# Kernel tuning notes

Hardware: AMD Instinct MI355X
Metric: run time of the kernel (lower is better)

## Reference

```python
import jax, jax.numpy as jnp
import numpy as np

M_FEATS = 1536      # number of proposals (docstring: [M, K])
K_DIM = 128         # feature dim per docstring example
NUM_CLASSES = 16    # label vocabulary; torch.unique loop becomes a fixed class sweep


def setup_inputs() -> dict:
    key = jax.random.key(0)
    k1, k2 = jax.random.split(key)
    features = jax.random.normal(k1, (M_FEATS, K_DIM), dtype=jnp.float32)
    labels = jax.random.randint(k2, (M_FEATS,), 0, NUM_CLASSES, dtype=jnp.int32)
    # ious all ones -> keep = (ious >= 0.5) is all-True, so the boolean filter is identity
    ious = jnp.ones((M_FEATS,), dtype=jnp.float32)
    return {"features": features, "labels": labels, "ious": ious}


def reference(features, labels, ious):
    # reweight_func='none' -> coef = ones_like(ious); keep mask is all-True by construction
    coef = jnp.ones_like(ious)
    # similarity [M, M]; coef broadcasts over columns, matching `similarity * coef` in torch
    sim = jnp.matmul(features, features.T) * coef[None, :]
    m = sim.shape[0]
    eye = jnp.eye(m, dtype=sim.dtype)
    # ground set term: logdet(similarity + 0.5 I)  (mask_ground is all ones)
    ground = jnp.linalg.slogdet(sim + 0.5 * eye)[1]

    # Per-label logdet of the submatrix S_c + 0.5 I_{n_c}. Instead of extracting a
    # variable-size submatrix (not jit-able), embed it in a full [M, M] matrix that is
    # block-diagonal: class block = S_c + 0.5 I, off-class diagonal = 1. Its logdet
    # equals logdet(S_c + 0.5 I). Absent classes give identity -> logdet 0, matching
    # torch.unique skipping them.
    onehot = (labels[:, None] == jnp.arange(NUM_CLASSES, dtype=labels.dtype)[None, :])
    onehot = onehot.astype(sim.dtype)  # [M, C]

    def class_logdet(mask):  # mask: [M] 0/1 indicator for one class
        A = sim * (mask[:, None] * mask[None, :]) + jnp.diag(0.5 * mask + (1.0 - mask))
        return jnp.linalg.slogdet(A)[1]

    per_class = jax.vmap(class_logdet)(onehot.T)  # [C]
    loss = jnp.sum(per_class) - ground
    return loss  # scalar; .mean() of a scalar is itself
```

## Files before the change

kernel.cpp:

```cpp
#include <hip/hip_runtime.h>
#include <math.h>


#define M_FEATS 1536
#define K_DIM 128
#define NUM_CLASSES 16
#define GRAM_ELEMS (K_DIM * K_DIM)
#define SENT 0x13579BDF
#define MP 104
#define ALD 132
#define WS 24

typedef short bf16x8 __attribute__((ext_vector_type(8)));
typedef float f32x4 __attribute__((ext_vector_type(4)));

__device__ __forceinline__ short f2bf(float x) {
    unsigned u = __float_as_uint(x);
    u += 0x7FFFu + ((u >> 16) & 1u);
    return (short)(u >> 16);
}

__device__ __forceinline__ float chol128_mfma(
    const int t, const float* __restrict__ Agram, float* __restrict__ strip,
    short* __restrict__ Whl, float* __restrict__ logp)
{
    const int wave = t >> 6, lane = t & 63, ln = lane & 15, quad = lane >> 4;

    f32x4 acc[2][8];
#pragma unroll
    for (int x = 0; x < 2; ++x)
#pragma unroll
        for (int tc = 0; tc < 8; ++tc)
            acc[x][tc] = (f32x4){0.f, 0.f, 0.f, 0.f};

#pragma unroll 1
    for (int s = 0; s < 16; ++s) {
        const int k = 8 * s;

        const int sb = s >> 1, sw = sb >> 1, sx = sb & 1, sq = (s & 1) * 2;
        if (wave == sw && (quad == sq || quad == sq + 1)) {
            const int qrel = quad - sq;
            const int rbase = (sw * 2 + sx) * 16 + quad * 4;
            if (sx == 0) {
#pragma unroll
                for (int tc = 0; tc < 8; ++tc)
#pragma unroll
                    for (int rr = 0; rr < 4; ++rr)
                        strip[(qrel * 4 + rr) * 128 + tc * 16 + ln] =
                            Agram[(rbase + rr) * ALD + tc * 16 + ln] - acc[0][tc][rr];
            } else {
#pragma unroll
                for (int tc = 0; tc < 8; ++tc)
#pragma unroll
                    for (int rr = 0; rr < 4; ++rr)
                        strip[(qrel * 4 + rr) * 128 + tc * 16 + ln] =
                            Agram[(rbase + rr) * ALD + tc * 16 + ln] - acc[1][tc][rr];
            }
        }
        __syncthreads();

        if (t < K_DIM) {
            float D[8][8];
#pragma unroll
            for (int r = 0; r < 8; ++r) {
                float4 d0 = *(const float4*)(strip + r * 128 + k);
                float4 d1 = *(const float4*)(strip + r * 128 + k + 4);
                D[r][0] = d0.x; D[r][1] = d0.y; D[r][2] = d0.z; D[r][3] = d0.w;
                D[r][4] = d1.x; D[r][5] = d1.y; D[r][6] = d1.z; D[r][7] = d1.w;
            }
            float a[8];
#pragma unroll
            for (int c = 0; c < 8; ++c) a[c] = strip[c * 128 + t];

            float L[8][8], ic[8];
            float prod = 1.0f;
#pragma unroll
            for (int c = 0; c < 8; ++c) {
                float v = D[c][c];
#pragma unroll
                for (int m = 0; m < c; ++m) v = fmaf(-L[c][m], L[c][m], v);
                prod *= v;
                ic[c] = rsqrtf(v);
#pragma unroll
                for (int r = c + 1; r < 8; ++r) {
                    float x = D[r][c];
#pragma unroll
                    for (int m = 0; m < c; ++m) x = fmaf(-L[r][m], L[c][m], x);
                    L[r][c] = x * ic[c];
                }
            }
            if (t == 0) logp[s] = prod;

            float w[8];
#pragma unroll
            for (int c = 0; c < 8; ++c) {
                float x = a[c];
#pragma unroll
                for (int m = 0; m < c; ++m) x = fmaf(-L[c][m], w[m], x);
                w[c] = x * ic[c];
            }
            if (t < k) {
#pragma unroll
                for (int c = 0; c < 8; ++c) w[c] = 0.f;
            }

            unsigned uh[4], ul[4];
#pragma unroll
            for (int j = 0; j < 4; ++j) {
                const float w0 = w[2 * j], w1 = w[2 * j + 1];
                const unsigned h0 = (unsigned short)f2bf(w0);
                const unsigned h1 = (unsigned short)f2bf(w1);
                const float f0 = __uint_as_float(h0 << 16);
                const float f1 = __uint_as_float(h1 << 16);
                const unsigned l0 = (unsigned short)f2bf(w0 - f0);
                const unsigned l1 = (unsigned short)f2bf(w1 - f1);
                uh[j] = (h1 << 16) | h0;
                ul[j] = (l1 << 16) | l0;
            }
            *(int4*)(Whl + t * WS) =
                make_int4((int)uh[0], (int)uh[1], (int)uh[2], (int)uh[3]);
            *(int4*)(Whl + t * WS + 8) =
                make_int4((int)ul[0], (int)ul[1], (int)ul[2], (int)ul[3]);
        }
        __syncthreads();

        const int live = 8 * (s + 1);
        const bool live0 = ((wave * 2 + 0) * 16 + 16) > live;
        const bool live1 = ((wave * 2 + 1) * 16 + 16) > live;
        if (live0 | live1) {
            const bf16x8 z = {};
            const short* a0p = Whl + (((wave * 2 + 0) * 16 + ln) * WS) + (quad & 1) * 8;
            const short* a1p = Whl + (((wave * 2 + 1) * 16 + ln) * WS) + (quad & 1) * 8;
            bf16x8 a0 = *(const bf16x8*)a0p;
            bf16x8 a1 = *(const bf16x8*)a1p;
            a0 = (quad < 2) ? a0 : z;
            a1 = (quad < 2) ? a1 : z;
#pragma unroll
            for (int tc = 0; tc < 8; ++tc) {
                if ((tc * 16 + 16) <= live) continue;
                const short* bp = Whl + (tc * 16 + ln) * WS;
                bf16x8 bh = *(const bf16x8*)(bp);
                bf16x8 bl = *(const bf16x8*)(bp + 8);
                bh = (quad < 2) ? bh : z;
                bl = (quad < 2) ? bl : z;
                if (live0) {
                    acc[0][tc] = __builtin_amdgcn_mfma_f32_16x16x32_bf16(
                        a0, bh, acc[0][tc], 0, 0, 0);
                    acc[0][tc] = __builtin_amdgcn_mfma_f32_16x16x32_bf16(
                        a0, bl, acc[0][tc], 0, 0, 0);
                }
                if (live1) {
                    acc[1][tc] = __builtin_amdgcn_mfma_f32_16x16x32_bf16(
                        a1, bh, acc[1][tc], 0, 0, 0);
                    acc[1][tc] = __builtin_amdgcn_mfma_f32_16x16x32_bf16(
                        a1, bl, acc[1][tc], 0, 0, 0);
                }
            }
        }
    }

    float ls = 0.0f;
    if (t == 0) {
#pragma unroll
        for (int ss = 0; ss < 16; ++ss) ls += logf(logp[ss]);
    }
    return ls;
}

__global__ __launch_bounds__(256, 1) void fused_kernel(
    const float* __restrict__ f, const int* __restrict__ labels,
    float* __restrict__ groundG, float* __restrict__ ldet,
    int* __restrict__ flagG, int* __restrict__ flag3,
    float* __restrict__ out)
{
    __shared__ int cnt;
    __shared__ int list[M_FEATS];
    __shared__ __align__(16) short FT[K_DIM * MP];
    __shared__ __align__(16) float Agram[K_DIM * ALD];
    __shared__ __align__(16) float strip[8 * 128];
    __shared__ __align__(16) short Whl[K_DIM * WS];
    __shared__ float logp[16];

    const int b = blockIdx.x;
    const int t = threadIdx.x;

    if (b < NUM_CLASSES) {
        const int cls = b;
        if (t == 0) cnt = 0;
        __syncthreads();
        {
            const int lane = t & 63;
            const unsigned long long ltmask = (lane == 63)
                ? 0x7FFFFFFFFFFFFFFFull : ((1ull << lane) - 1ull);
#pragma unroll
            for (int it = 0; it < M_FEATS / 256; ++it) {
                const int i = it * 256 + t;
                const bool pred = (labels[i] == cls);
                const unsigned long long mask = __ballot(pred);
                int base = 0;
                if (lane == 0 && mask)
                    base = atomicAdd(&cnt, __popcll(mask));
                base = __shfl(base, 0);
                if (pred)
                    list[base + __popcll(mask & ltmask)] = i;
            }
        }
        __syncthreads();
        const int n = cnt;

        const int wave = t >> 6, lane = t & 63, ln = lane & 15, quad = lane >> 4;
        const int mlane = t & 31, cgrp = t >> 5;

        f32x4 acc[2][8];
#pragma unroll
        for (int x = 0; x < 2; ++x)
#pragma unroll
            for (int tc = 0; tc < 8; ++tc)
                acc[x][tc] = (f32x4){0.f, 0.f, 0.f, 0.f};

        const int nchunks = (n + 95) / 96;
        for (int ch = 0; ch < nchunks; ++ch) {
            const int cb = ch * 96;
#pragma unroll
            for (int it = 0; it < 12; ++it) {
                const int m = (it % 3) * 32 + mlane;
                const int cgp = (it / 3) * 8 + cgrp;
                const int gm = cb + m;
                float4 v = make_float4(0.f, 0.f, 0.f, 0.f);
                if (gm < n) {
                    const int src = list[gm];
                    v = *(const float4*)(f + (size_t)src * K_DIM + cgp * 4);
                }
                FT[(cgp * 4 + 0) * MP + m] = f2bf(v.x);
                FT[(cgp * 4 + 1) * MP + m] = f2bf(v.y);
                FT[(cgp * 4 + 2) * MP + m] = f2bf(v.z);
                FT[(cgp * 4 + 3) * MP + m] = f2bf(v.w);
            }
            __syncthreads();
#pragma unroll
            for (int kc = 0; kc < 3; ++kc) {
                const int kb = kc * 32 + quad * 8;
                bf16x8 a0 = *(const bf16x8*)(FT + ((wave * 2 + 0) * 16 + ln) * MP + kb);
                bf16x8 a1 = *(const bf16x8*)(FT + ((wave * 2 + 1) * 16 + ln) * MP + kb);
#pragma unroll
                for (int tc = 0; tc < 8; ++tc) {
                    bf16x8 bb = *(const bf16x8*)(FT + (tc * 16 + ln) * MP + kb);
                    acc[0][tc] = __builtin_amdgcn_mfma_f32_16x16x32_bf16(
                        a0, bb, acc[0][tc], 0, 0, 0);
                    acc[1][tc] = __builtin_amdgcn_mfma_f32_16x16x32_bf16(
                        a1, bb, acc[1][tc], 0, 0, 0);
                }
            }
            __syncthreads();
        }

#pragma unroll
        for (int x = 0; x < 2; ++x)
#pragma unroll
            for (int tc = 0; tc < 8; ++tc)
#pragma unroll
                for (int rr = 0; rr < 4; ++rr) {
                    const int row = (wave * 2 + x) * 16 + quad * 4 + rr;
                    const int col = tc * 16 + ln;
                    const float v = acc[x][tc][rr];
                    Agram[row * ALD + col] = v;
                    unsafeAtomicAdd(&groundG[row * K_DIM + col], v);
                }
        __syncthreads();
        if (t == 0)
            __hip_atomic_store(&flagG[cls], SENT, __ATOMIC_RELEASE,
                               __HIP_MEMORY_SCOPE_AGENT);

        if (t < K_DIM) Agram[t * ALD + t] += 0.5f;
        __syncthreads();

        float ls = chol128_mfma(t, Agram, strip, Whl, logp);

        if (t == 0) {
            ldet[cls] = ls;
            __hip_atomic_store(&flag3[cls], SENT, __ATOMIC_RELEASE,
                               __HIP_MEMORY_SCOPE_AGENT);
        }
        return;
    }

    if (t < NUM_CLASSES)
        while (__hip_atomic_load(&flagG[t], __ATOMIC_ACQUIRE,
                                 __HIP_MEMORY_SCOPE_AGENT) != SENT)
            __builtin_amdgcn_s_sleep(2);
    __syncthreads();

#pragma unroll
    for (int j = 0; j < 16; ++j) {
        const int idx = j * 256 + t;
        const int row = idx >> 5, c4 = idx & 31;
        *(float4*)(Agram + row * ALD + c4 * 4) =
            *(const float4*)(groundG + (size_t)idx * 4);
    }
    __syncthreads();
    if (t < K_DIM) Agram[t * ALD + t] += 0.5f;
    __syncthreads();

    float ls = chol128_mfma(t, Agram, strip, Whl, logp);

    if (t < NUM_CLASSES)
        while (__hip_atomic_load(&flag3[t], __ATOMIC_ACQUIRE,
                                 __HIP_MEMORY_SCOPE_AGENT) != SENT)
            __builtin_amdgcn_s_sleep(2);
    __syncthreads();

    if (t == 0) {
        float total = 1920.0f * 0.6931471805599453f - ls;
#pragma unroll
        for (int c = 0; c < NUM_CLASSES; ++c) total += ldet[c];
        out[0] = total;
    }
}

extern "C" void kernel_launch(void* const* d_in, const int* in_sizes, int n_in,
                              void* d_out, int out_size, void* d_ws, size_t ws_size,
                              hipStream_t stream)
{
    const float* features = (const float*)d_in[0];
    const int* labels = (const int*)d_in[1];

    float* groundG = (float*)d_ws;
    float* ldetp   = groundG + GRAM_ELEMS;
    int* flagG     = (int*)(ldetp + NUM_CLASSES);
    int* flag3     = flagG + NUM_CLASSES;

    fused_kernel<<<NUM_CLASSES + 1, 256, 0, stream>>>(
        features, labels, groundG, ldetp, flagG, flag3, (float*)d_out);
}
```

Baseline: 100.6 us.

## Run Cholesky directly on register-resident Gram accumulators with negated-B trailing updates

The Gram matrix is no longer staged in a shared-memory Agram array. The Cholesky factorization now starts from the MFMA accumulators themselves and subtracts trailing updates by multiplying against stored negated bf16 hi/lo panels, which are sign-flipped with XOR. The strip is transposed to a column-major 8-wide layout so panel and column reads become float4 vector loads, and the ground block loads groundG straight into registers. This removes the Agram round-trips, the extra barriers and one subtraction per element, at the cost of a larger Whl buffer and indexed register access to the diagonal, which may spill to scratch.

```diff
diff --git a/kernel.cpp b/kernel.cpp
--- a/kernel.cpp
+++ b/kernel.cpp
@@ -8,8 +8,7 @@
 #define GRAM_ELEMS (K_DIM * K_DIM)
 #define SENT 0x13579BDF
 #define MP 104
-#define ALD 132
-#define WS 24
+#define WS2 40
 
 typedef short bf16x8 __attribute__((ext_vector_type(8)));
 typedef float f32x4 __attribute__((ext_vector_type(4)));
@@ -20,19 +19,12 @@
     return (short)(u >> 16);
 }
 
-__device__ __forceinline__ float chol128_mfma(
-    const int t, const float* __restrict__ Agram, float* __restrict__ strip,
+__device__ __forceinline__ float chol128_acc(
+    const int t, f32x4 acc[2][8], float* __restrict__ strip,
     short* __restrict__ Whl, float* __restrict__ logp)
 {
     const int wave = t >> 6, lane = t & 63, ln = lane & 15, quad = lane >> 4;
 
-    f32x4 acc[2][8];
-#pragma unroll
-    for (int x = 0; x < 2; ++x)
-#pragma unroll
-        for (int tc = 0; tc < 8; ++tc)
-            acc[x][tc] = (f32x4){0.f, 0.f, 0.f, 0.f};
-
 #pragma unroll 1
     for (int s = 0; s < 16; ++s) {
         const int k = 8 * s;
@@ -40,37 +32,25 @@
         const int sb = s >> 1, sw = sb >> 1, sx = sb & 1, sq = (s & 1) * 2;
         if (wave == sw && (quad == sq || quad == sq + 1)) {
             const int qrel = quad - sq;
-            const int rbase = (sw * 2 + sx) * 16 + quad * 4;
-            if (sx == 0) {
-#pragma unroll
-                for (int tc = 0; tc < 8; ++tc)
-#pragma unroll
-                    for (int rr = 0; rr < 4; ++rr)
-                        strip[(qrel * 4 + rr) * 128 + tc * 16 + ln] =
-                            Agram[(rbase + rr) * ALD + tc * 16 + ln] - acc[0][tc][rr];
-            } else {
-#pragma unroll
-                for (int tc = 0; tc < 8; ++tc)
-#pragma unroll
-                    for (int rr = 0; rr < 4; ++rr)
-                        strip[(qrel * 4 + rr) * 128 + tc * 16 + ln] =
-                            Agram[(rbase + rr) * ALD + tc * 16 + ln] - acc[1][tc][rr];
-            }
+#pragma unroll
+            for (int tc = 0; tc < 8; ++tc)
+                *(f32x4*)(strip + (tc * 16 + ln) * 8 + qrel * 4) =
+                    sx ? acc[1][tc] : acc[0][tc];
         }
         __syncthreads();
 
         if (t < K_DIM) {
             float D[8][8];
 #pragma unroll
-            for (int r = 0; r < 8; ++r) {
-                float4 d0 = *(const float4*)(strip + r * 128 + k);
-                float4 d1 = *(const float4*)(strip + r * 128 + k + 4);
-                D[r][0] = d0.x; D[r][1] = d0.y; D[r][2] = d0.z; D[r][3] = d0.w;
-                D[r][4] = d1.x; D[r][5] = d1.y; D[r][6] = d1.z; D[r][7] = d1.w;
-            }
-            float a[8];
-#pragma unroll
-            for (int c = 0; c < 8; ++c) a[c] = strip[c * 128 + t];
+            for (int c = 0; c < 8; ++c) {
+                float4 d0 = *(const float4*)(strip + (k + c) * 8);
+                float4 d1 = *(const float4*)(strip + (k + c) * 8 + 4);
+                D[0][c] = d0.x; D[1][c] = d0.y; D[2][c] = d0.z; D[3][c] = d0.w;
+                D[4][c] = d1.x; D[5][c] = d1.y; D[6][c] = d1.z; D[7][c] = d1.w;
+            }
+            float4 av0 = *(const float4*)(strip + t * 8);
+            float4 av1 = *(const float4*)(strip + t * 8 + 4);
+            float a[8] = {av0.x, av0.y, av0.z, av0.w, av1.x, av1.y, av1.z, av1.w};
 
             float L[8][8], ic[8];
             float prod = 1.0f;
@@ -117,10 +97,13 @@
                 uh[j] = (h1 << 16) | h0;
                 ul[j] = (l1 << 16) | l0;
             }
-            *(int4*)(Whl + t * WS) =
-                make_int4((int)uh[0], (int)uh[1], (int)uh[2], (int)uh[3]);
-            *(int4*)(Whl + t * WS + 8) =
-                make_int4((int)ul[0], (int)ul[1], (int)ul[2], (int)ul[3]);
+            short* wp = Whl + t * WS2;
+            *(int4*)(wp) = make_int4((int)uh[0], (int)uh[1], (int)uh[2], (int)uh[3]);
+            *(int4*)(wp + 8) = make_int4((int)ul[0], (int)ul[1], (int)ul[2], (int)ul[3]);
+            *(int4*)(wp + 16) = make_int4((int)(uh[0] ^ 0x80008000u), (int)(uh[1] ^ 0x80008000u),
+                                          (int)(uh[2] ^ 0x80008000u), (int)(uh[3] ^ 0x80008000u));
+            *(int4*)(wp + 24) = make_int4((int)(ul[0] ^ 0x80008000u), (int)(ul[1] ^ 0x80008000u),
+                                          (int)(ul[2] ^ 0x80008000u), (int)(ul[3] ^ 0x80008000u));
         }
         __syncthreads();
 
@@ -129,18 +112,16 @@
         const bool live1 = ((wave * 2 + 1) * 16 + 16) > live;
         if (live0 | live1) {
             const bf16x8 z = {};
-            const short* a0p = Whl + (((wave * 2 + 0) * 16 + ln) * WS) + (quad & 1) * 8;
-            const short* a1p = Whl + (((wave * 2 + 1) * 16 + ln) * WS) + (quad & 1) * 8;
-            bf16x8 a0 = *(const bf16x8*)a0p;
-            bf16x8 a1 = *(const bf16x8*)a1p;
+            bf16x8 a0 = *(const bf16x8*)(Whl + (((wave * 2 + 0) * 16 + ln) * WS2) + (quad & 1) * 8);
+            bf16x8 a1 = *(const bf16x8*)(Whl + (((wave * 2 + 1) * 16 + ln) * WS2) + (quad & 1) * 8);
             a0 = (quad < 2) ? a0 : z;
             a1 = (quad < 2) ? a1 : z;
 #pragma unroll
             for (int tc = 0; tc < 8; ++tc) {
                 if ((tc * 16 + 16) <= live) continue;
-                const short* bp = Whl + (tc * 16 + ln) * WS;
-                bf16x8 bh = *(const bf16x8*)(bp);
-                bf16x8 bl = *(const bf16x8*)(bp + 8);
+                const short* bp = Whl + (tc * 16 + ln) * WS2;
+                bf16x8 bh = *(const bf16x8*)(bp + 16);
+                bf16x8 bl = *(const bf16x8*)(bp + 24);
                 bh = (quad < 2) ? bh : z;
                 bl = (quad < 2) ? bl : z;
                 if (live0) {
@@ -176,20 +157,26 @@
     __shared__ int cnt;
     __shared__ int list[M_FEATS];
     __shared__ __align__(16) short FT[K_DIM * MP];
-    __shared__ __align__(16) float Agram[K_DIM * ALD];
     __shared__ __align__(16) float strip[8 * 128];
-    __shared__ __align__(16) short Whl[K_DIM * WS];
+    __shared__ __align__(16) short Whl[K_DIM * WS2];
     __shared__ float logp[16];
 
     const int b = blockIdx.x;
     const int t = threadIdx.x;
+    const int wave = t >> 6, lane = t & 63, ln = lane & 15, quad = lane >> 4;
+
+    f32x4 acc[2][8];
+#pragma unroll
+    for (int x = 0; x < 2; ++x)
+#pragma unroll
+        for (int tc = 0; tc < 8; ++tc)
+            acc[x][tc] = (f32x4){0.f, 0.f, 0.f, 0.f};
 
     if (b < NUM_CLASSES) {
         const int cls = b;
         if (t == 0) cnt = 0;
         __syncthreads();
         {
-            const int lane = t & 63;
             const unsigned long long ltmask = (lane == 63)
                 ? 0x7FFFFFFFFFFFFFFFull : ((1ull << lane) - 1ull);
 #pragma unroll
@@ -208,16 +195,7 @@
         __syncthreads();
         const int n = cnt;
 
-        const int wave = t >> 6, lane = t & 63, ln = lane & 15, quad = lane >> 4;
         const int mlane = t & 31, cgrp = t >> 5;
-
-        f32x4 acc[2][8];
-#pragma unroll
-        for (int x = 0; x < 2; ++x)
-#pragma unroll
-            for (int tc = 0; tc < 8; ++tc)
-                acc[x][tc] = (f32x4){0.f, 0.f, 0.f, 0.f};
-
         const int nchunks = (n + 95) / 96;
         for (int ch = 0; ch < nchunks; ++ch) {
             const int cb = ch * 96;
@@ -262,19 +240,21 @@
                 for (int rr = 0; rr < 4; ++rr) {
                     const int row = (wave * 2 + x) * 16 + quad * 4 + rr;
                     const int col = tc * 16 + ln;
-                    const float v = acc[x][tc][rr];
-                    Agram[row * ALD + col] = v;
-                    unsafeAtomicAdd(&groundG[row * K_DIM + col], v);
+                    unsafeAtomicAdd(&groundG[row * K_DIM + col], acc[x][tc][rr]);
                 }
         __syncthreads();
         if (t == 0)
             __hip_atomic_store(&flagG[cls], SENT, __ATOMIC_RELEASE,
                                __HIP_MEMORY_SCOPE_AGENT);
 
-        if (t < K_DIM) Agram[t * ALD + t] += 0.5f;
-        __syncthreads();
-
-        float ls = chol128_mfma(t, Agram, strip, Whl, logp);
+#pragma unroll
+        for (int x = 0; x < 2; ++x) {
+            const int tcd = wave * 2 + x;
+            const int rrd = ln - quad * 4;
+            if (rrd >= 0 && rrd < 4) acc[x][tcd][rrd] += 0.5f;
+        }
+
+        float ls = chol128_acc(t, acc, strip, Whl, logp);
 
         if (t == 0) {
             ldet[cls] = ls;
@@ -291,17 +271,23 @@
     __syncthreads();
 
 #pragma unroll
-    for (int j = 0; j < 16; ++j) {
-        const int idx = j * 256 + t;
-        const int row = idx >> 5, c4 = idx & 31;
-        *(float4*)(Agram + row * ALD + c4 * 4) =
-            *(const float4*)(groundG + (size_t)idx * 4);
-    }
-    __syncthreads();
-    if (t < K_DIM) Agram[t * ALD + t] += 0.5f;
-    __syncthreads();
-
-    float ls = chol128_mfma(t, Agram, strip, Whl, logp);
+    for (int x = 0; x < 2; ++x)
+#pragma unroll
+        for (int tc = 0; tc < 8; ++tc)
+#pragma unroll
+            for (int rr = 0; rr < 4; ++rr) {
+                const int row = (wave * 2 + x) * 16 + quad * 4 + rr;
+                const int col = tc * 16 + ln;
+                acc[x][tc][rr] = groundG[row * K_DIM + col];
+            }
+#pragma unroll
+    for (int x = 0; x < 2; ++x) {
+        const int tcd = wave * 2 + x;
+        const int rrd = ln - quad * 4;
+        if (rrd >= 0 && rrd < 4) acc[x][tcd][rrd] += 0.5f;
+    }
+
+    float ls = chol128_acc(t, acc, strip, Whl, logp);
 
     if (t < NUM_CLASSES)
         while (__hip_atomic_load(&flag3[t], __ATOMIC_ACQUIRE,
```

After: 128.6 us. 27.9% more time.
